# Kernel tuning notes

Measured on AMD Instinct MI355X. Metric: run time of the kernel, lower is better.

Reference implementation:

```python
import jax, jax.numpy as jnp
from jax import lax
import numpy as np

DIM = 512
NUM_HEADS = 8
SR = 2


def setup_inputs() -> dict:
    key = jax.random.key(0)
    ks = jax.random.split(key, 7)
    B, H, W = 4, 64, 64
    N = H * W
    C = DIM
    s = 0.02
    return {
        "x": jax.random.normal(ks[0], (B, N, C), dtype=jnp.float32),
        "q_w": jax.random.normal(ks[1], (C, C), dtype=jnp.float32) * s,
        "kv_w": jax.random.normal(ks[2], (2 * C, C), dtype=jnp.float32) * s,
        "sr_w": jax.random.normal(ks[3], (C, C, SR, SR), dtype=jnp.float32) * s,
        "sr_b": jax.random.normal(ks[4], (C,), dtype=jnp.float32) * s,
        "proj_w": jax.random.normal(ks[5], (C, C), dtype=jnp.float32) * s,
        "proj_b": jax.random.normal(ks[6], (C,), dtype=jnp.float32) * s,
        "H": H,
        "W": W,
    }


def reference(x, q_w, kv_w, sr_w, sr_b, proj_w, proj_b, H, W):
    B, N, C = x.shape
    nh = NUM_HEADS
    hd = C // nh
    scale = hd ** -0.5

    # q projection: [B, nh, N, hd]
    q = (x @ q_w.T).reshape(B, N, nh, hd).transpose(0, 2, 1, 3)

    # spatial reduction via strided conv (kernel=stride=SR)
    x_ = x.transpose(0, 2, 1).reshape(B, C, H, W)
    x_ = lax.conv_general_dilated(
        x_, sr_w, window_strides=(SR, SR), padding="VALID",
        dimension_numbers=("NCHW", "OIHW", "NCHW"),
    ) + sr_b[None, :, None, None]
    Nk = (H // SR) * (W // SR)
    x_ = x_.reshape(B, C, Nk).transpose(0, 2, 1)  # [B, Nk, C]

    # kv projection: [2, B, nh, Nk, hd]
    kv = (x_ @ kv_w.T).reshape(B, Nk, 2, nh, hd).transpose(2, 0, 3, 1, 4)
    k, v = kv[0], kv[1]

    attn = jax.nn.softmax(jnp.einsum("bhnd,bhmd->bhnm", q, k) * scale, axis=-1)
    out = jnp.einsum("bhnm,bhmd->bhnd", attn, v)  # [B, nh, N, hd]
    out = out.transpose(0, 2, 1, 3).reshape(B, N, C)
    return out @ proj_w.T + proj_b
```

## Files before the change

kernel.cpp:

```cpp
#include <hip/hip_runtime.h>


typedef __attribute__((ext_vector_type(8)))  short short8;
typedef __attribute__((ext_vector_type(8)))  unsigned short ushort8;
typedef __attribute__((ext_vector_type(4)))  float floatx4;
typedef __attribute__((ext_vector_type(16))) float floatx16;

__device__ inline unsigned short bf16r(float f) {
    union { float f; unsigned u; } v; v.f = f;
    unsigned r = v.u + 0x7fffu + ((v.u >> 16) & 1u);
    return (unsigned short)(r >> 16);
}

__device__ inline unsigned long long pack4ull(float4 v) {
    return (unsigned long long)bf16r(v.x)
         | ((unsigned long long)bf16r(v.y) << 16)
         | ((unsigned long long)bf16r(v.z) << 32)
         | ((unsigned long long)bf16r(v.w) << 48);
}

__device__ inline ushort8 pack8(float4 a, float4 b) {
    ushort8 o;
    o[0] = bf16r(a.x); o[1] = bf16r(a.y); o[2] = bf16r(a.z); o[3] = bf16r(a.w);
    o[4] = bf16r(b.x); o[5] = bf16r(b.y); o[6] = bf16r(b.z); o[7] = bf16r(b.w);
    return o;
}

__device__ inline void gl_lds16(const void* g, void* l) {
    __builtin_amdgcn_global_load_lds(
        (const __attribute__((address_space(1))) unsigned int*)g,
        (__attribute__((address_space(3))) unsigned int*)l, 16, 0, 0);
}

__global__ __launch_bounds__(256)
void prep(const float* __restrict__ x,  const float* __restrict__ qw,
          const float* __restrict__ kvw, const float* __restrict__ srw,
          const float* __restrict__ pw,
          unsigned short* __restrict__ xb,  unsigned short* __restrict__ qwb,
          unsigned short* __restrict__ kvwb, unsigned short* __restrict__ srwb,
          unsigned short* __restrict__ pwb, unsigned short* __restrict__ xrb) {
    const int bid = blockIdx.x;
    if (bid < 2048) {
        const int id = bid * 256 + threadIdx.x;
        const int cq = id & 127, m = id >> 7;
        const int c0 = cq * 4;
        const int b = m >> 10, rem = m & 1023;
        const int oi = rem >> 5, oj = rem & 31;
        const int n00 = oi * 128 + oj * 2;
        const float* bp = x + ((size_t)(b * 4096 + n00)) * 512 + c0;
        const float4 r00 = *(const float4*)bp;
        const float4 r01 = *(const float4*)(bp + 512);
        const float4 r10 = *(const float4*)(bp + 64 * 512);
        const float4 r11 = *(const float4*)(bp + 65 * 512);
        const unsigned long long w00 = pack4ull(r00), w01 = pack4ull(r01),
                                 w10 = pack4ull(r10), w11 = pack4ull(r11);
        unsigned short* xo = xb + ((size_t)(b * 4096 + n00)) * 512 + c0;
        *(unsigned long long*)(xo)            = w00;
        *(unsigned long long*)(xo + 512)      = w01;
        *(unsigned long long*)(xo + 64 * 512) = w10;
        *(unsigned long long*)(xo + 65 * 512) = w11;
        unsigned short* xd = xrb + (size_t)m * 2048 + c0 * 4;
        #pragma unroll
        for (int j = 0; j < 4; ++j) {
            const unsigned long long e =
                  ((w00 >> (16 * j)) & 0xffffull)
                | (((w01 >> (16 * j)) & 0xffffull) << 16)
                | (((w10 >> (16 * j)) & 0xffffull) << 32)
                | (((w11 >> (16 * j)) & 0xffffull) << 48);
            *(unsigned long long*)(xd + j * 4) = e;
        }
    } else {
        const int b2 = bid - 2048;
        const float* src; unsigned short* dst; int off; float sc = 1.f;
        if (b2 < 128)      { src = qw;  dst = qwb;  off = b2 * 256;
                             sc = 0.18033688011112042f;  }
        else if (b2 < 384) { src = kvw; dst = kvwb; off = (b2 - 128) * 256; }
        else if (b2 < 896) { src = srw; dst = srwb; off = (b2 - 384) * 256; }
        else               { src = pw;  dst = pwb;  off = (b2 - 896) * 256; }
        const int idx = off + threadIdx.x;
        float4 a = *(const float4*)(src + (size_t)idx * 8);
        float4 bq = *(const float4*)(src + (size_t)idx * 8 + 4);
        a.x *= sc; a.y *= sc; a.z *= sc; a.w *= sc;
        bq.x *= sc; bq.y *= sc; bq.z *= sc; bq.w *= sc;
        *(ushort8*)(dst + (size_t)idx * 8) = pack8(a, bq);
    }
}

__device__ __forceinline__ void g_stage(
        const unsigned short* __restrict__ A, const unsigned short* __restrict__ B,
        int K, int bm, int bn, int k0, int t,
        unsigned short* AsB, unsigned short* BsB) {
    #pragma unroll
    for (int i = 0; i < 4; ++i) {
        const int c = i * 256 + t;
        const int r = c >> 3, ch = c & 7;
        gl_lds16(A + (size_t)(bm + r) * K + k0 + ((ch ^ (r & 7)) * 8), AsB + c * 8);
    }
    #pragma unroll
    for (int i = 0; i < 4; ++i) {
        const int c = i * 256 + t;
        const int r = c >> 3, ch = c & 7;
        gl_lds16(B + (size_t)(bn + r) * K + k0 + ((ch ^ (r & 7)) * 8), BsB + c * 8);
    }
}

__device__ __forceinline__ void g_comp(
        const unsigned short* AsB, const unsigned short* BsB,
        int lq, int quad, int wrow, int wcol, floatx4 (&acc)[4][4]) {
    #pragma unroll
    for (int kc = 0; kc < 2; ++kc) {
        short8 bfq[4];
        #pragma unroll
        for (int ni = 0; ni < 4; ++ni) {
            const int r = wcol + ni * 16 + lq;
            bfq[ni] = *(const short8*)&BsB[r * 64 + (((kc * 4 + quad) ^ (r & 7)) * 8)];
        }
        #pragma unroll
        for (int mi = 0; mi < 4; ++mi) {
            const int r = wrow + mi * 16 + lq;
            const short8 af = *(const short8*)&AsB[r * 64 + (((kc * 4 + quad) ^ (r & 7)) * 8)];
            #pragma unroll
            for (int ni = 0; ni < 4; ++ni)
                acc[mi][ni] = __builtin_amdgcn_mfma_f32_16x16x32_bf16(
                    af, bfq[ni], acc[mi][ni], 0, 0, 0);
        }
    }
}

__device__ __forceinline__ void g_run(
        const unsigned short* __restrict__ A, const unsigned short* __restrict__ B,
        int K, int bm, int bn, int t, int lq, int quad, int wrow, int wcol,
        unsigned short (&As)[2][128 * 64], unsigned short (&Bs)[2][128 * 64],
        floatx4 (&acc)[4][4]) {
    g_stage(A, B, K, bm, bn, 0, t, As[0], Bs[0]);
    __syncthreads();
    const int nk = K >> 6;
    for (int ks = 0; ks < nk; ++ks) {
        const int cur = ks & 1;
        if (ks + 1 < nk)
            g_stage(A, B, K, bm, bn, (ks + 1) * 64, t, As[cur ^ 1], Bs[cur ^ 1]);
        __builtin_amdgcn_s_setprio(1);
        g_comp(As[cur], Bs[cur], lq, quad, wrow, wcol, acc);
        __builtin_amdgcn_s_setprio(0);
        if (ks + 1 < nk) __syncthreads();
    }
}

__global__ __launch_bounds__(256)
void gemm_qc(const unsigned short* __restrict__ xb, const unsigned short* __restrict__ qwb,
             const unsigned short* __restrict__ xrb, const unsigned short* __restrict__ srwb,
             const float* __restrict__ sr_b,
             unsigned short* __restrict__ qb, unsigned short* __restrict__ xsrb) {
    __shared__ unsigned short As[2][128 * 64];
    __shared__ unsigned short Bs[2][128 * 64];
    const int t = threadIdx.x;
    const int w = t >> 6, l = t & 63;
    const int lq = l & 15, quad = l >> 4;
    const int wrow = (w >> 1) * 64, wcol = (w & 1) * 64;
    const int bx = blockIdx.x;
    const unsigned short *A, *B; int K, bm; const float* bias; unsigned short* C;
    if (bx < 128) { A = xb;  B = qwb;  K = 512;  bm = bx * 128;         bias = nullptr; C = qb;   }
    else          { A = xrb; B = srwb; K = 2048; bm = (bx - 128) * 128; bias = sr_b;    C = xsrb; }
    const int bn = blockIdx.y * 128;

    floatx4 acc[4][4];
    #pragma unroll
    for (int mi = 0; mi < 4; ++mi)
        #pragma unroll
        for (int ni = 0; ni < 4; ++ni) acc[mi][ni] = (floatx4){0.f, 0.f, 0.f, 0.f};

    g_run(A, B, K, bm, bn, t, lq, quad, wrow, wcol, As, Bs, acc);

    #pragma unroll
    for (int ni = 0; ni < 4; ++ni) {
        const int col = bn + wcol + ni * 16 + lq;
        const float bv = bias ? bias[col] : 0.f;
        #pragma unroll
        for (int mi = 0; mi < 4; ++mi) {
            const int row0 = bm + wrow + mi * 16 + quad * 4;
            unsigned own[4], mg[4];
            #pragma unroll
            for (int r = 0; r < 4; ++r) own[r] = bf16r(acc[mi][ni][r] + bv);
            #pragma unroll
            for (int r = 0; r < 4; ++r) {
                const unsigned pt = __shfl_xor(own[r], 1);
                mg[r] = (lq & 1) ? (pt | (own[r] << 16)) : (own[r] | (pt << 16));
            }
            const int colb = bn + wcol + ni * 16 + (lq & ~1);
            const int rb = (lq & 1) * 2;
            *(unsigned*)(C + (size_t)(row0 + rb)     * 512 + colb) = mg[rb];
            *(unsigned*)(C + (size_t)(row0 + rb + 1) * 512 + colb) = mg[rb + 1];
        }
    }
}

__global__ __launch_bounds__(256)
void gemm_kv(const unsigned short* __restrict__ kvwb, const unsigned short* __restrict__ xsrb,
             unsigned short* __restrict__ Kb, unsigned short* __restrict__ Vt) {
    __shared__ unsigned short As[2][128 * 64];
    __shared__ unsigned short Bs[2][128 * 64];
    const int t = threadIdx.x;
    const int w = t >> 6, l = t & 63;
    const int lq = l & 15, quad = l >> 4;
    const int wrow = (w >> 1) * 64, wcol = (w & 1) * 64;
    const int id = blockIdx.x;
    const bool isK = id < 128;
    const int id2 = isK ? id : id - 128;
    const unsigned short* A = isK ? kvwb : xsrb;
    const unsigned short* B = isK ? xsrb : kvwb + (size_t)512 * 512;
    const int bm = isK ? (id2 & 3) * 128 : (id2 >> 2) * 128;
    const int bn = isK ? (id2 >> 2) * 128 : (id2 & 3) * 128;

    floatx4 acc[4][4];
    #pragma unroll
    for (int mi = 0; mi < 4; ++mi)
        #pragma unroll
        for (int ni = 0; ni < 4; ++ni) acc[mi][ni] = (floatx4){0.f, 0.f, 0.f, 0.f};

    g_run(A, B, 512, bm, bn, t, lq, quad, wrow, wcol, As, Bs, acc);

    #pragma unroll
    for (int ni = 0; ni < 4; ++ni) {
        const int col = bn + wcol + ni * 16 + lq;
        #pragma unroll
        for (int mi = 0; mi < 4; ++mi) {
            const int row0 = bm + wrow + mi * 16 + quad * 4;
            unsigned long long wv = 0;
            #pragma unroll
            for (int r = 0; r < 4; ++r)
                wv |= (unsigned long long)bf16r(acc[mi][ni][r]) << (16 * r);
            if (isK) {
                const int kb = col >> 10, key = col & 1023;
                const int h = row0 >> 6, d0 = row0 & 63;
                *(unsigned long long*)(Kb +
                    (((size_t)(kb * 8 + h)) * 1024 + key) * 64 + d0) = wv;
            } else {
                const int kb = row0 >> 10, key0 = row0 & 1023;
                const int h = col >> 6, d = col & 63;
                *(unsigned long long*)(Vt +
                    (((size_t)(kb * 8 + h)) * 64 + d) * 1024 + key0) = wv;
            }
        }
    }
}

__global__ __launch_bounds__(256)
void gemm_proj(const unsigned short* __restrict__ attb, const unsigned short* __restrict__ pwb,
               const float* __restrict__ pb, float* __restrict__ out) {
    __shared__ unsigned short As[2][128 * 64];
    __shared__ unsigned short Bs[2][128 * 64];
    const int t = threadIdx.x;
    const int w = t >> 6, l = t & 63;
    const int lq = l & 15, quad = l >> 4;
    const int wrow = (w >> 1) * 64, wcol = (w & 1) * 64;
    const int bm = blockIdx.x * 128, bn = blockIdx.y * 128;

    floatx4 acc[4][4];
    #pragma unroll
    for (int mi = 0; mi < 4; ++mi)
        #pragma unroll
        for (int ni = 0; ni < 4; ++ni) acc[mi][ni] = (floatx4){0.f, 0.f, 0.f, 0.f};

    g_run(attb, pwb, 512, bm, bn, t, lq, quad, wrow, wcol, As, Bs, acc);

    #pragma unroll
    for (int ni = 0; ni < 4; ++ni) {
        const int col = bn + wcol + ni * 16 + lq;
        const float bv = pb[col];
        #pragma unroll
        for (int mi = 0; mi < 4; ++mi) {
            const int row0 = bm + wrow + mi * 16 + quad * 4;
            #pragma unroll
            for (int r = 0; r < 4; ++r)
                out[(size_t)(row0 + r) * 512 + col] = acc[mi][ni][r] + bv;
        }
    }
}

#define KS2 72
#define VS2 136

__global__ __launch_bounds__(256)
void attn_mfma32(const unsigned short* __restrict__ qb,
                 const unsigned short* __restrict__ Kb,
                 const unsigned short* __restrict__ Vt,
                 unsigned short* __restrict__ out) {
    __shared__ unsigned short Ks[128 * KS2];
    __shared__ unsigned short Vs[64 * VS2];

    const int t = threadIdx.x;
    const int w = t >> 6;
    const int lane = t & 63;
    const int m32 = lane & 31;
    const int sig = lane >> 5;
    const int hw = blockIdx.x;
    const int lid = (hw & 7) * 128 + (hw >> 3);
    const int bh = lid >> 5;
    const int n0 = (lid & 31) * 128;
    const int b = bh >> 3, h = bh & 7;

    short8 qf[4];
    {
        const unsigned short* qrow =
            qb + ((size_t)(b * 4096 + n0 + w * 32 + m32)) * 512 + h * 64;
        #pragma unroll
        for (int kc = 0; kc < 4; ++kc)
            qf[kc] = *(const short8*)(qrow + kc * 16 + sig * 8);
    }

    float l_own = 0.f;
    floatx16 O0, O1;
    #pragma unroll
    for (int i = 0; i < 16; ++i) { O0[i] = 0.f; O1[i] = 0.f; }

    const unsigned short* Kg = Kb + (size_t)bh * 1024 * 64;
    const unsigned short* Vg = Vt + (size_t)bh * 64 * 1024;
    const int srow = t >> 2;
    const int sdb  = (t & 3) * 16;

    for (int kt2 = 0; kt2 < 8; ++kt2) {
        __syncthreads();
        {
            #pragma unroll
            for (int i = 0; i < 2; ++i) {
                const int row = i * 64 + srow;
                const unsigned short* src =
                    Kg + ((size_t)(kt2 * 128 + row)) * 64 + sdb;
                *(ushort8*)&Ks[row * KS2 + sdb]     = *(const ushort8*)src;
                *(ushort8*)&Ks[row * KS2 + sdb + 8] = *(const ushort8*)(src + 8);
            }
        }
        {
            #pragma unroll
            for (int i = 0; i < 2; ++i) {
                const int colb = i * 64 + sdb;
                const unsigned short* src =
                    Vg + (size_t)srow * 1024 + kt2 * 128 + colb;
                *(ushort8*)&Vs[srow * VS2 + colb]     = *(const ushort8*)src;
                *(ushort8*)&Vs[srow * VS2 + colb + 8] = *(const ushort8*)(src + 8);
            }
        }
        __syncthreads();

        #pragma unroll
        for (int half = 0; half < 2; ++half) {
            const int kof = half * 64;

            floatx16 st0, st1;
            #pragma unroll
            for (int i = 0; i < 16; ++i) { st0[i] = 0.f; st1[i] = 0.f; }
            __builtin_amdgcn_s_setprio(1);
            #pragma unroll
            for (int kc = 0; kc < 4; ++kc) {
                const short8 a0 = *(const short8*)
                    &Ks[(kof + m32) * KS2 + kc * 16 + sig * 8];
                st0 = __builtin_amdgcn_mfma_f32_32x32x16_bf16(a0, qf[kc], st0, 0, 0, 0);
                const short8 a1 = *(const short8*)
                    &Ks[(kof + 32 + m32) * KS2 + kc * 16 + sig * 8];
                st1 = __builtin_amdgcn_mfma_f32_32x32x16_bf16(a1, qf[kc], st1, 0, 0, 0);
            }
            __builtin_amdgcn_s_setprio(0);

            uint2 E[2][4];
            #pragma unroll
            for (int g = 0; g < 2; ++g) {
                #pragma unroll
                for (int qd = 0; qd < 4; ++qd) {
                    const float p0 = __builtin_amdgcn_exp2f(g ? st1[qd * 4 + 0] : st0[qd * 4 + 0]);
                    const float p1 = __builtin_amdgcn_exp2f(g ? st1[qd * 4 + 1] : st0[qd * 4 + 1]);
                    const float p2 = __builtin_amdgcn_exp2f(g ? st1[qd * 4 + 2] : st0[qd * 4 + 2]);
                    const float p3 = __builtin_amdgcn_exp2f(g ? st1[qd * 4 + 3] : st0[qd * 4 + 3]);
                    E[g][qd].x = __builtin_amdgcn_perm(
                        __float_as_uint(p1), __float_as_uint(p0), 0x07060302u);
                    E[g][qd].y = __builtin_amdgcn_perm(
                        __float_as_uint(p3), __float_as_uint(p2), 0x07060302u);
                    l_own += (p0 + p1) + (p2 + p3);
                }
            }

            __builtin_amdgcn_s_setprio(1);
            #pragma unroll
            for (int kc = 0; kc < 4; ++kc) {
                const int g = kc >> 1, qlo = (kc & 1) * 2;
                unsigned ax = E[g][qlo].x, bx_ = E[g][qlo + 1].x;
                unsigned ay = E[g][qlo].y, by_ = E[g][qlo + 1].y;
                asm("v_permlane32_swap_b32 %0, %1" : "+v"(ax), "+v"(bx_));
                asm("v_permlane32_swap_b32 %0, %1" : "+v"(ay), "+v"(by_));
                uint4 fr; fr.x = ax; fr.y = ay; fr.z = bx_; fr.w = by_;
                const short8 pa = *(const short8*)&fr;
                const short8 v0 = *(const short8*)
                    &Vs[m32 * VS2 + kof + kc * 16 + sig * 8];
                O0 = __builtin_amdgcn_mfma_f32_32x32x16_bf16(pa, v0, O0, 0, 0, 0);
                const short8 v1 = *(const short8*)
                    &Vs[(32 + m32) * VS2 + kof + kc * 16 + sig * 8];
                O1 = __builtin_amdgcn_mfma_f32_32x32x16_bf16(pa, v1, O1, 0, 0, 0);
            }
            __builtin_amdgcn_s_setprio(0);
        }
    }

    l_own += __shfl_xor(l_own, 32);
    const float inv = 1.0f / l_own;

    float fo0[16], fo1[16];
    #pragma unroll
    for (int r = 0; r < 16; ++r) {
        const float li = __shfl(inv, ((r & 3) + 8 * (r >> 2)) + 4 * sig);
        fo0[r] = O0[r] * li;
        fo1[r] = O1[r] * li;
    }

    #pragma unroll
    for (int gd = 0; gd < 2; ++gd) {
        unsigned mg[16];
        #pragma unroll
        for (int r = 0; r < 16; ++r) {
            const unsigned own = bf16r(gd ? fo1[r] : fo0[r]);
            const unsigned pt = __shfl_xor(own, 1);
            mg[r] = (m32 & 1) ? (pt | (own << 16)) : (own | (pt << 16));
        }
        if ((m32 & 1) == gd) {
            const int colb = h * 64 + gd * 32 + (m32 & ~1);
            #pragma unroll
            for (int r = 0; r < 16; ++r) {
                const int qrow = (r & 3) + 8 * (r >> 2) + 4 * sig;
                const size_t row = (size_t)(b * 4096 + n0 + w * 32 + qrow);
                *(unsigned*)(out + row * 512 + colb) = mg[r];
            }
        }
    }
}

extern "C" void kernel_launch(void* const* d_in, const int* in_sizes, int n_in,
                              void* d_out, int out_size, void* d_ws, size_t ws_size,
                              hipStream_t stream) {
    const float* x      = (const float*)d_in[0];
    const float* q_w    = (const float*)d_in[1];
    const float* kv_w   = (const float*)d_in[2];
    const float* sr_w   = (const float*)d_in[3];
    const float* sr_b   = (const float*)d_in[4];
    const float* proj_w = (const float*)d_in[5];
    const float* proj_b = (const float*)d_in[6];
    float* out = (float*)d_out;

    unsigned short* xb   = (unsigned short*)d_ws;
    unsigned short* attb = xb;
    unsigned short* qb   = xb   + (size_t)16384 * 512;
    unsigned short* xrb  = qb   + (size_t)16384 * 512;
    unsigned short* xsrb = xrb  + (size_t)4096 * 2048;
    unsigned short* qwb  = xsrb + (size_t)4096 * 512;
    unsigned short* kvwb = qwb  + (size_t)512 * 512;
    unsigned short* srwb = kvwb + (size_t)1024 * 512;
    unsigned short* pwb  = srwb + (size_t)512 * 2048;
    unsigned short* Kb   = pwb  + (size_t)512 * 512;
    unsigned short* Vt   = Kb   + (size_t)32 * 1024 * 64;

    const dim3 blk(256);

    prep<<<3072, blk, 0, stream>>>(x, q_w, kv_w, sr_w, proj_w,
                                   xb, qwb, kvwb, srwb, pwb, xrb);

    gemm_qc<<<dim3(160, 4), blk, 0, stream>>>(xb, qwb, xrb, srwb, sr_b, qb, xsrb);

    gemm_kv<<<256, blk, 0, stream>>>(kvwb, xsrb, Kb, Vt);

    attn_mfma32<<<1024, blk, 0, stream>>>(qb, Kb, Vt, attb);

    gemm_proj<<<dim3(128, 4), blk, 0, stream>>>(attb, pwb, proj_b, out);
}
```

Baseline: 225.6 us.

## Single-buffer qc/proj GEMMs, reorder long-K blocks first, halve kv tile width

The qc and proj GEMMs move from double-buffered to single-buffered LDS tiles (32 KB instead of 64 KB), which allows more resident blocks per CU. The price is that global loads no longer overlap compute within a block. gemm_qc now places the long-K (2048) conv blocks at the lowest block indices so they are scheduled first, reducing tail imbalance. gemm_kv switches to 128x64 tiles with 512 blocks, improving wave coverage on a small GEMM at the cost of lower per-block data reuse.

```diff
diff --git a/kernel.cpp b/kernel.cpp
--- a/kernel.cpp
+++ b/kernel.cpp
@@ -86,26 +86,26 @@
     }
 }
 
-__device__ __forceinline__ void g_stage(
+__device__ __forceinline__ void g_stage128(
         const unsigned short* __restrict__ A, const unsigned short* __restrict__ B,
         int K, int bm, int bn, int k0, int t,
-        unsigned short* AsB, unsigned short* BsB) {
+        unsigned short* As, unsigned short* Bs) {
     #pragma unroll
     for (int i = 0; i < 4; ++i) {
         const int c = i * 256 + t;
         const int r = c >> 3, ch = c & 7;
-        gl_lds16(A + (size_t)(bm + r) * K + k0 + ((ch ^ (r & 7)) * 8), AsB + c * 8);
+        gl_lds16(A + (size_t)(bm + r) * K + k0 + ((ch ^ (r & 7)) * 8), As + c * 8);
     }
     #pragma unroll
     for (int i = 0; i < 4; ++i) {
         const int c = i * 256 + t;
         const int r = c >> 3, ch = c & 7;
-        gl_lds16(B + (size_t)(bn + r) * K + k0 + ((ch ^ (r & 7)) * 8), BsB + c * 8);
-    }
-}
-
-__device__ __forceinline__ void g_comp(
-        const unsigned short* AsB, const unsigned short* BsB,
+        gl_lds16(B + (size_t)(bn + r) * K + k0 + ((ch ^ (r & 7)) * 8), Bs + c * 8);
+    }
+}
+
+__device__ __forceinline__ void g_comp128(
+        const unsigned short* As, const unsigned short* Bs,
         int lq, int quad, int wrow, int wcol, floatx4 (&acc)[4][4]) {
     #pragma unroll
     for (int kc = 0; kc < 2; ++kc) {
@@ -113,12 +113,12 @@
         #pragma unroll
         for (int ni = 0; ni < 4; ++ni) {
             const int r = wcol + ni * 16 + lq;
-            bfq[ni] = *(const short8*)&BsB[r * 64 + (((kc * 4 + quad) ^ (r & 7)) * 8)];
+            bfq[ni] = *(const short8*)&Bs[r * 64 + (((kc * 4 + quad) ^ (r & 7)) * 8)];
         }
         #pragma unroll
         for (int mi = 0; mi < 4; ++mi) {
             const int r = wrow + mi * 16 + lq;
-            const short8 af = *(const short8*)&AsB[r * 64 + (((kc * 4 + quad) ^ (r & 7)) * 8)];
+            const short8 af = *(const short8*)&As[r * 64 + (((kc * 4 + quad) ^ (r & 7)) * 8)];
             #pragma unroll
             for (int ni = 0; ni < 4; ++ni)
                 acc[mi][ni] = __builtin_amdgcn_mfma_f32_16x16x32_bf16(
@@ -127,22 +127,19 @@
     }
 }
 
-__device__ __forceinline__ void g_run(
+__device__ __forceinline__ void g_run128(
         const unsigned short* __restrict__ A, const unsigned short* __restrict__ B,
         int K, int bm, int bn, int t, int lq, int quad, int wrow, int wcol,
-        unsigned short (&As)[2][128 * 64], unsigned short (&Bs)[2][128 * 64],
+        unsigned short (&As)[128 * 64], unsigned short (&Bs)[128 * 64],
         floatx4 (&acc)[4][4]) {
-    g_stage(A, B, K, bm, bn, 0, t, As[0], Bs[0]);
-    __syncthreads();
     const int nk = K >> 6;
     for (int ks = 0; ks < nk; ++ks) {
-        const int cur = ks & 1;
-        if (ks + 1 < nk)
-            g_stage(A, B, K, bm, bn, (ks + 1) * 64, t, As[cur ^ 1], Bs[cur ^ 1]);
+        __syncthreads();
+        g_stage128(A, B, K, bm, bn, ks * 64, t, As, Bs);
+        __syncthreads();
         __builtin_amdgcn_s_setprio(1);
-        g_comp(As[cur], Bs[cur], lq, quad, wrow, wcol, acc);
+        g_comp128(As, Bs, lq, quad, wrow, wcol, acc);
         __builtin_amdgcn_s_setprio(0);
-        if (ks + 1 < nk) __syncthreads();
     }
 }
 
@@ -151,16 +148,16 @@
              const unsigned short* __restrict__ xrb, const unsigned short* __restrict__ srwb,
              const float* __restrict__ sr_b,
              unsigned short* __restrict__ qb, unsigned short* __restrict__ xsrb) {
-    __shared__ unsigned short As[2][128 * 64];
-    __shared__ unsigned short Bs[2][128 * 64];
+    __shared__ unsigned short As[128 * 64];
+    __shared__ unsigned short Bs[128 * 64];
     const int t = threadIdx.x;
     const int w = t >> 6, l = t & 63;
     const int lq = l & 15, quad = l >> 4;
     const int wrow = (w >> 1) * 64, wcol = (w & 1) * 64;
     const int bx = blockIdx.x;
     const unsigned short *A, *B; int K, bm; const float* bias; unsigned short* C;
-    if (bx < 128) { A = xb;  B = qwb;  K = 512;  bm = bx * 128;         bias = nullptr; C = qb;   }
-    else          { A = xrb; B = srwb; K = 2048; bm = (bx - 128) * 128; bias = sr_b;    C = xsrb; }
+    if (bx < 32) { A = xrb; B = srwb; K = 2048; bm = bx * 128;        bias = sr_b;    C = xsrb; }
+    else         { A = xb;  B = qwb;  K = 512;  bm = (bx - 32) * 128; bias = nullptr; C = qb;   }
     const int bn = blockIdx.y * 128;
 
     floatx4 acc[4][4];
@@ -169,7 +166,7 @@
         #pragma unroll
         for (int ni = 0; ni < 4; ++ni) acc[mi][ni] = (floatx4){0.f, 0.f, 0.f, 0.f};
 
-    g_run(A, B, K, bm, bn, t, lq, quad, wrow, wcol, As, Bs, acc);
+    g_run128(A, B, K, bm, bn, t, lq, quad, wrow, wcol, As, Bs, acc);
 
     #pragma unroll
     for (int ni = 0; ni < 4; ++ni) {
@@ -195,35 +192,120 @@
 }
 
 __global__ __launch_bounds__(256)
-void gemm_kv(const unsigned short* __restrict__ kvwb, const unsigned short* __restrict__ xsrb,
-             unsigned short* __restrict__ Kb, unsigned short* __restrict__ Vt) {
-    __shared__ unsigned short As[2][128 * 64];
-    __shared__ unsigned short Bs[2][128 * 64];
+void gemm_proj(const unsigned short* __restrict__ attb, const unsigned short* __restrict__ pwb,
+               const float* __restrict__ pb, float* __restrict__ out) {
+    __shared__ unsigned short As[128 * 64];
+    __shared__ unsigned short Bs[128 * 64];
     const int t = threadIdx.x;
     const int w = t >> 6, l = t & 63;
     const int lq = l & 15, quad = l >> 4;
     const int wrow = (w >> 1) * 64, wcol = (w & 1) * 64;
+    const int bm = blockIdx.x * 128, bn = blockIdx.y * 128;
+
+    floatx4 acc[4][4];
+    #pragma unroll
+    for (int mi = 0; mi < 4; ++mi)
+        #pragma unroll
+        for (int ni = 0; ni < 4; ++ni) acc[mi][ni] = (floatx4){0.f, 0.f, 0.f, 0.f};
+
+    g_run128(attb, pwb, 512, bm, bn, t, lq, quad, wrow, wcol, As, Bs, acc);
+
+    #pragma unroll
+    for (int ni = 0; ni < 4; ++ni) {
+        const int col = bn + wcol + ni * 16 + lq;
+        const float bv = pb[col];
+        #pragma unroll
+        for (int mi = 0; mi < 4; ++mi) {
+            const int row0 = bm + wrow + mi * 16 + quad * 4;
+            #pragma unroll
+            for (int r = 0; r < 4; ++r)
+                out[(size_t)(row0 + r) * 512 + col] = acc[mi][ni][r] + bv;
+        }
+    }
+}
+
+__device__ __forceinline__ void g_stage64(
+        const unsigned short* __restrict__ A, const unsigned short* __restrict__ B,
+        int K, int bm, int bn, int k0, int t,
+        unsigned short* AsB, unsigned short* BsB) {
+    #pragma unroll
+    for (int i = 0; i < 4; ++i) {
+        const int c = i * 256 + t;
+        const int r = c >> 3, ch = c & 7;
+        gl_lds16(A + (size_t)(bm + r) * K + k0 + ((ch ^ (r & 7)) * 8), AsB + c * 8);
+    }
+    #pragma unroll
+    for (int i = 0; i < 2; ++i) {
+        const int c = i * 256 + t;
+        const int r = c >> 3, ch = c & 7;
+        gl_lds16(B + (size_t)(bn + r) * K + k0 + ((ch ^ (r & 7)) * 8), BsB + c * 8);
+    }
+}
+
+__device__ __forceinline__ void g_comp64(
+        const unsigned short* AsB, const unsigned short* BsB,
+        int lq, int quad, int wrow, floatx4 (&acc)[2][4]) {
+    short8 bf[2][4];
+    #pragma unroll
+    for (int kc = 0; kc < 2; ++kc)
+        #pragma unroll
+        for (int ni = 0; ni < 4; ++ni) {
+            const int r = ni * 16 + lq;
+            bf[kc][ni] = *(const short8*)&BsB[r * 64 + (((kc * 4 + quad) ^ (r & 7)) * 8)];
+        }
+    #pragma unroll
+    for (int mi = 0; mi < 2; ++mi) {
+        const int r = wrow + mi * 16 + lq;
+        #pragma unroll
+        for (int kc = 0; kc < 2; ++kc) {
+            const short8 af = *(const short8*)&AsB[r * 64 + (((kc * 4 + quad) ^ (r & 7)) * 8)];
+            #pragma unroll
+            for (int ni = 0; ni < 4; ++ni)
+                acc[mi][ni] = __builtin_amdgcn_mfma_f32_16x16x32_bf16(
+                    af, bf[kc][ni], acc[mi][ni], 0, 0, 0);
+        }
+    }
+}
+
+__global__ __launch_bounds__(256)
+void gemm_kv(const unsigned short* __restrict__ kvwb, const unsigned short* __restrict__ xsrb,
+             unsigned short* __restrict__ Kb, unsigned short* __restrict__ Vt) {
+    __shared__ unsigned short As[2][128 * 64];
+    __shared__ unsigned short Bs[2][64 * 64];
+    const int t = threadIdx.x;
+    const int w = t >> 6, l = t & 63;
+    const int lq = l & 15, quad = l >> 4;
+    const int wrow = w * 32;
     const int id = blockIdx.x;
-    const bool isK = id < 128;
-    const int id2 = isK ? id : id - 128;
+    const bool isK = id < 256;
     const unsigned short* A = isK ? kvwb : xsrb;
     const unsigned short* B = isK ? xsrb : kvwb + (size_t)512 * 512;
-    const int bm = isK ? (id2 & 3) * 128 : (id2 >> 2) * 128;
-    const int bn = isK ? (id2 >> 2) * 128 : (id2 & 3) * 128;
-
-    floatx4 acc[4][4];
-    #pragma unroll
-    for (int mi = 0; mi < 4; ++mi)
+    const int bm = isK ? (id & 3) * 128 : ((id - 256) >> 3) * 128;
+    const int bn = isK ? (id >> 2) * 64 : ((id - 256) & 7) * 64;
+
+    floatx4 acc[2][4];
+    #pragma unroll
+    for (int mi = 0; mi < 2; ++mi)
         #pragma unroll
         for (int ni = 0; ni < 4; ++ni) acc[mi][ni] = (floatx4){0.f, 0.f, 0.f, 0.f};
 
-    g_run(A, B, 512, bm, bn, t, lq, quad, wrow, wcol, As, Bs, acc);
+    g_stage64(A, B, 512, bm, bn, 0, t, As[0], Bs[0]);
+    __syncthreads();
+    for (int ks = 0; ks < 8; ++ks) {
+        const int cur = ks & 1;
+        if (ks + 1 < 8)
+            g_stage64(A, B, 512, bm, bn, (ks + 1) * 64, t, As[cur ^ 1], Bs[cur ^ 1]);
+        __builtin_amdgcn_s_setprio(1);
+        g_comp64(As[cur], Bs[cur], lq, quad, wrow, acc);
+        __builtin_amdgcn_s_setprio(0);
+        if (ks + 1 < 8) __syncthreads();
+    }
 
     #pragma unroll
     for (int ni = 0; ni < 4; ++ni) {
-        const int col = bn + wcol + ni * 16 + lq;
-        #pragma unroll
-        for (int mi = 0; mi < 4; ++mi) {
+        const int col = bn + ni * 16 + lq;
+        #pragma unroll
+        for (int mi = 0; mi < 2; ++mi) {
             const int row0 = bm + wrow + mi * 16 + quad * 4;
             unsigned long long wv = 0;
             #pragma unroll
@@ -240,39 +322,6 @@
                 *(unsigned long long*)(Vt +
                     (((size_t)(kb * 8 + h)) * 64 + d) * 1024 + key0) = wv;
             }
-        }
-    }
-}
-
-__global__ __launch_bounds__(256)
-void gemm_proj(const unsigned short* __restrict__ attb, const unsigned short* __restrict__ pwb,
-               const float* __restrict__ pb, float* __restrict__ out) {
-    __shared__ unsigned short As[2][128 * 64];
-    __shared__ unsigned short Bs[2][128 * 64];
-    const int t = threadIdx.x;
-    const int w = t >> 6, l = t & 63;
-    const int lq = l & 15, quad = l >> 4;
-    const int wrow = (w >> 1) * 64, wcol = (w & 1) * 64;
-    const int bm = blockIdx.x * 128, bn = blockIdx.y * 128;
-
-    floatx4 acc[4][4];
-    #pragma unroll
-    for (int mi = 0; mi < 4; ++mi)
-        #pragma unroll
-        for (int ni = 0; ni < 4; ++ni) acc[mi][ni] = (floatx4){0.f, 0.f, 0.f, 0.f};
-
-    g_run(attb, pwb, 512, bm, bn, t, lq, quad, wrow, wcol, As, Bs, acc);
-
-    #pragma unroll
-    for (int ni = 0; ni < 4; ++ni) {
-        const int col = bn + wcol + ni * 16 + lq;
-        const float bv = pb[col];
-        #pragma unroll
-        for (int mi = 0; mi < 4; ++mi) {
-            const int row0 = bm + wrow + mi * 16 + quad * 4;
-            #pragma unroll
-            for (int r = 0; r < 4; ++r)
-                out[(size_t)(row0 + r) * 512 + col] = acc[mi][ni][r] + bv;
         }
     }
 }
@@ -462,7 +511,7 @@
 
     gemm_qc<<<dim3(160, 4), blk, 0, stream>>>(xb, qwb, xrb, srwb, sr_b, qb, xsrb);
 
-    gemm_kv<<<256, blk, 0, stream>>>(kvwb, xsrb, Kb, Vt);
+    gemm_kv<<<512, blk, 0, stream>>>(kvwb, xsrb, Kb, Vt);
 
     attn_mfma32<<<1024, blk, 0, stream>>>(qb, Kb, Vt, attb);
 
```

Result: faster. 215.6 us (-4.4%).
